# Optimization experiments

Hardware: AMD Instinct MI355X
Metric: run time of the kernel (lower is better)

The kernel has to match this reference:

```python
import jax, jax.numpy as jnp
import numpy as np


def setup_inputs() -> dict:
    key = jax.random.key(0)
    k1, k2 = jax.random.split(key)
    B, HW, C, M, P = 8, 4096, 1024, 32, 512
    feature_map = jax.random.normal(k1, (B, HW, C), dtype=jnp.float32)
    # normalized (y, x) coords in [0,1], as produced by mask.nonzero()/[H,W]
    point_coords = jax.random.uniform(k2, (B, M, P, 2), dtype=jnp.float32)
    return {"feature_map": feature_map, "point_coords": point_coords}


def reference(feature_map, point_coords):
    # feature_map: [B, H*W, C]; point_coords: [B, M, P, 2] as (y_norm, x_norm).
    B, HW, C = feature_map.shape
    h = w = int(np.sqrt(HW))
    # torch flips coords to (x, y); grid_sample(align_corners=True) maps
    # grid g = 2*coord-1 to pixel coord*(size-1).
    y = point_coords[..., 0] * (h - 1)  # [B, M, P]
    x = point_coords[..., 1] * (w - 1)
    x0f = jnp.floor(x)
    y0f = jnp.floor(y)
    wx = (x - x0f)[..., None]  # [B, M, P, 1]
    wy = (y - y0f)[..., None]
    ix0 = jnp.clip(x0f.astype(jnp.int32), 0, w - 1)
    ix1 = jnp.clip(ix0 + 1, 0, w - 1)
    iy0 = jnp.clip(y0f.astype(jnp.int32), 0, h - 1)
    iy1 = jnp.clip(iy0 + 1, 0, h - 1)

    def gather(iy, ix):
        idx = (iy * w + ix).reshape(B, -1)  # [B, M*P]
        g = jnp.take_along_axis(feature_map, idx[:, :, None], axis=1)  # [B, M*P, C]
        return g.reshape(B, iy.shape[1], iy.shape[2], C)

    f00 = gather(iy0, ix0)
    f01 = gather(iy0, ix1)
    f10 = gather(iy1, ix0)
    f11 = gather(iy1, ix1)
    # bilinear interpolation -> [B, M, P, C]
    sampled = (f00 * (1 - wx) * (1 - wy) + f01 * wx * (1 - wy)
               + f10 * (1 - wx) * wy + f11 * wx * wy)
    # AdaptiveAvgPool1d(1) over points, then transpose -> [B, M, 1, C]
    region_feat = jnp.mean(sampled, axis=2, keepdims=True)
    return region_feat
```

## Files before the change

kernel.cpp:

```cpp
#include <hip/hip_runtime.h>


#define NB 8
#define NM 32
#define NP 512
#define NC 1024
#define NH 64
#define NHW 4096

#define KC    128
#define NKC   (NHW / KC)
#define CPT   8
#define MT    8
#define CTILE 512
#define NCT   (NC / CTILE)
#define PF    4

__global__ __launch_bounds__(256) void scatter_w(
    const float* __restrict__ pc, float* __restrict__ W)
{
    int idx = blockIdx.x * 256 + threadIdx.x;
    int bm  = idx >> 9;
    int m   = bm & (NM - 1);
    int b   = bm >> 5;

    float2 c = ((const float2*)pc)[idx];
    float y = c.x * 63.0f;
    float x = c.y * 63.0f;
    float x0f = floorf(x), y0f = floorf(y);
    float wx = x - x0f, wy = y - y0f;
    int ix0 = min(max((int)x0f, 0), 63);
    int ix1 = min(ix0 + 1, 63);
    int iy0 = min(max((int)y0f, 0), 63);
    int iy1 = min(iy0 + 1, 63);
    float wx1 = 1.0f - wx, wy1 = 1.0f - wy;
    const float s = 1.0f / (float)NP;

    float* Wb = W + (size_t)b * (NHW * NM) + m;
    atomicAdd(Wb + ((iy0 * NH + ix0) * NM), wx1 * wy1 * s);
    atomicAdd(Wb + ((iy0 * NH + ix1) * NM), wx  * wy1 * s);
    atomicAdd(Wb + ((iy1 * NH + ix0) * NM), wx1 * wy  * s);
    atomicAdd(Wb + ((iy1 * NH + ix1) * NM), wx  * wy  * s);
}

__global__ __launch_bounds__(256, 2) void wgemm(
    const float* __restrict__ W, const float* __restrict__ F,
    float* __restrict__ P)
{
    __shared__ float sW[KC * NM];

    const int kc   = blockIdx.x;
    const int ct   = blockIdx.y;
    const int b    = blockIdx.z;
    const int tid  = threadIdx.x;
    const int mq   = tid >> 6;
    const int lane = tid & 63;
    const int c0   = ct * CTILE + lane * CPT;
    const int hw0  = kc * KC;

    {
        const float4* Wg = (const float4*)(W + ((size_t)b * NHW + hw0) * NM);
        float4* sW4 = (float4*)sW;
#pragma unroll
        for (int j = 0; j < 4; ++j)
            sW4[tid + 256 * j] = Wg[tid + 256 * j];
    }
    __syncthreads();

    const float4* __restrict__ Fb =
        (const float4*)(F + ((size_t)b * NHW + hw0) * NC + c0);
    const int fstride = NC / 4;

    float4 acc[MT][2];
#pragma unroll
    for (int m = 0; m < MT; ++m) {
        acc[m][0] = make_float4(0.f, 0.f, 0.f, 0.f);
        acc[m][1] = make_float4(0.f, 0.f, 0.f, 0.f);
    }

    float4 fbuf[PF][2];
#pragma unroll
    for (int j = 0; j < PF; ++j) {
        fbuf[j][0] = Fb[(size_t)j * fstride];
        fbuf[j][1] = Fb[(size_t)j * fstride + 1];
    }

    const float4* sWq = (const float4*)(sW + mq * MT);

    for (int i = 0; i < KC; i += PF) {
#pragma unroll
        for (int j = 0; j < PF; ++j) {
            const int s = i + j;
            float4 wa0 = sWq[(size_t)s * (NM / 4)];
            float4 wa1 = sWq[(size_t)s * (NM / 4) + 1];

            float4 f0 = fbuf[j][0];
            float4 f1 = fbuf[j][1];
            if (i + PF < KC) {
                fbuf[j][0] = Fb[(size_t)(s + PF) * fstride];
                fbuf[j][1] = Fb[(size_t)(s + PF) * fstride + 1];
            }

            const float wm[MT] = { wa0.x, wa0.y, wa0.z, wa0.w,
                                   wa1.x, wa1.y, wa1.z, wa1.w };
#pragma unroll
            for (int m = 0; m < MT; ++m) {
                float w = wm[m];
                acc[m][0].x = fmaf(w, f0.x, acc[m][0].x);
                acc[m][0].y = fmaf(w, f0.y, acc[m][0].y);
                acc[m][0].z = fmaf(w, f0.z, acc[m][0].z);
                acc[m][0].w = fmaf(w, f0.w, acc[m][0].w);
                acc[m][1].x = fmaf(w, f1.x, acc[m][1].x);
                acc[m][1].y = fmaf(w, f1.y, acc[m][1].y);
                acc[m][1].z = fmaf(w, f1.z, acc[m][1].z);
                acc[m][1].w = fmaf(w, f1.w, acc[m][1].w);
            }
        }
    }

    float* pb = P + (((size_t)kc * NB + b) * NM + mq * MT) * NC + c0;
#pragma unroll
    for (int mm = 0; mm < MT; ++mm) {
        ((float4*)(pb + (size_t)mm * NC))[0] = acc[mm][0];
        ((float4*)(pb + (size_t)mm * NC))[1] = acc[mm][1];
    }
}

__global__ __launch_bounds__(256) void reduce_p(
    const float* __restrict__ P, float* __restrict__ out)
{
    const int idx = blockIdx.x * 256 + threadIdx.x;
    const float4* p4 = (const float4*)P;
    const int stride = NB * NM * NC / 4;
    float4 s = make_float4(0.f, 0.f, 0.f, 0.f);
#pragma unroll
    for (int kc = 0; kc < NKC; ++kc) {
        float4 v = p4[(size_t)kc * stride + idx];
        s.x += v.x; s.y += v.y; s.z += v.z; s.w += v.w;
    }
    ((float4*)out)[idx] = s;
}

__global__ __launch_bounds__(256) void region_pool_direct(
    const float* __restrict__ fm, const float* __restrict__ pc,
    float* __restrict__ out)
{
    __shared__ int4   sIdx[NP];
    __shared__ float4 sWt[NP];
    const int bid = blockIdx.x;
    const int b   = bid >> 5;
    const int tid = threadIdx.x;
    const float2* pc2 = (const float2*)(pc + (size_t)bid * NP * 2);
    for (int p = tid; p < NP; p += 256) {
        float2 c = pc2[p];
        float y = c.x * 63.0f, x = c.y * 63.0f;
        float x0f = floorf(x), y0f = floorf(y);
        float wx = x - x0f, wy = y - y0f;
        int ix0 = min(max((int)x0f, 0), 63);
        int ix1 = min(ix0 + 1, 63);
        int iy0 = min(max((int)y0f, 0), 63);
        int iy1 = min(iy0 + 1, 63);
        sIdx[p] = make_int4((iy0 * NH + ix0) << 10, (iy0 * NH + ix1) << 10,
                            (iy1 * NH + ix0) << 10, (iy1 * NH + ix1) << 10);
        float wx1 = 1.0f - wx, wy1 = 1.0f - wy;
        sWt[p] = make_float4(wx1 * wy1, wx * wy1, wx1 * wy, wx * wy);
    }
    __syncthreads();
    const float* Fb = fm + (size_t)b * (NHW * NC) + tid * 4;
    float4 acc = make_float4(0.f, 0.f, 0.f, 0.f);
#pragma unroll 4
    for (int p = 0; p < NP; ++p) {
        int4 off = sIdx[p]; float4 w = sWt[p];
        float4 f00 = *(const float4*)(Fb + off.x);
        float4 f01 = *(const float4*)(Fb + off.y);
        float4 f10 = *(const float4*)(Fb + off.z);
        float4 f11 = *(const float4*)(Fb + off.w);
        acc.x = fmaf(w.x, f00.x, fmaf(w.y, f01.x, fmaf(w.z, f10.x, fmaf(w.w, f11.x, acc.x))));
        acc.y = fmaf(w.x, f00.y, fmaf(w.y, f01.y, fmaf(w.z, f10.y, fmaf(w.w, f11.y, acc.y))));
        acc.z = fmaf(w.x, f00.z, fmaf(w.y, f01.z, fmaf(w.z, f10.z, fmaf(w.w, f11.z, acc.z))));
        acc.w = fmaf(w.x, f00.w, fmaf(w.y, f01.w, fmaf(w.z, f10.w, fmaf(w.w, f11.w, acc.w))));
    }
    const float inv = 1.0f / (float)NP;
    ((float4*)(out + (size_t)bid * NC))[tid] =
        make_float4(acc.x * inv, acc.y * inv, acc.z * inv, acc.w * inv);
}

extern "C" void kernel_launch(void* const* d_in, const int* in_sizes, int n_in,
                              void* d_out, int out_size, void* d_ws, size_t ws_size,
                              hipStream_t stream) {
    const float* fm = (const float*)d_in[0];
    const float* pc = (const float*)d_in[1];
    float* out = (float*)d_out;

    const size_t wbytes = (size_t)NB * NHW * NM * sizeof(float);
    const size_t pbytes = (size_t)NKC * NB * NM * NC * sizeof(float);
    if (ws_size >= wbytes + pbytes) {
        float* W = (float*)d_ws;
        float* P = (float*)((char*)d_ws + wbytes);
        hipMemsetAsync(W, 0, wbytes, stream);
        scatter_w<<<(NB * NM * NP) / 256, 256, 0, stream>>>(pc, W);
        dim3 grid(NKC, NCT, NB);
        wgemm<<<grid, 256, 0, stream>>>(W, fm, P);
        reduce_p<<<(NB * NM * NC / 4) / 256, 256, 0, stream>>>(P, out);
    } else {
        region_pool_direct<<<NB * NM, 256, 0, stream>>>(fm, pc, out);
    }
}
```

Baseline: 250.3 us.

## Stage feature tiles in LDS with async global-to-LDS loads, double buffered

In the weighted-GEMM kernel, all four wavefronts of a block previously loaded the same feature rows straight from global memory into registers. Each block now copies chunks of eight feature rows into a shared double-buffered LDS tile using the global_load_lds builtin, with each wavefront fetching two rows. The copy of the next chunk overlaps compute on the current one. Columns are now interleaved (lane*4 and 256+lane*4) so the LDS reads are contiguous. This removes the redundant global/L1 traffic, at the cost of a block barrier per chunk and reliance on correct wait handling for the async LDS loads.

```diff
diff --git a/kernel.cpp b/kernel.cpp
--- a/kernel.cpp
+++ b/kernel.cpp
@@ -8,13 +8,13 @@
 #define NH 64
 #define NHW 4096
 
-#define KC    128
-#define NKC   (NHW / KC)
-#define CPT   8
-#define MT    8
-#define CTILE 512
-#define NCT   (NC / CTILE)
-#define PF    4
+#define KC     128
+#define NKC    (NHW / KC)
+#define MT     8
+#define CTILE  512
+#define NCT    (NC / CTILE)
+#define G      8
+#define NCHUNK (KC / G)
 
 __global__ __launch_bounds__(256) void scatter_w(
     const float* __restrict__ pc, float* __restrict__ W)
@@ -43,11 +43,30 @@
     atomicAdd(Wb + ((iy1 * NH + ix1) * NM), wx  * wy  * s);
 }
 
+__device__ __forceinline__ void dma_rows(const float* src, float* dstBase,
+                                         int lane)
+{
+#pragma unroll
+    for (int jj = 0; jj < 2; ++jj) {
+        const float* s0 = src + jj * NC + lane * 4;
+        const float* s1 = src + jj * NC + 256 + lane * 4;
+        float* d0 = dstBase + jj * CTILE + lane * 4;
+        float* d1 = dstBase + jj * CTILE + 256 + lane * 4;
+        __builtin_amdgcn_global_load_lds(
+            (const __attribute__((address_space(1))) void*)s0,
+            (__attribute__((address_space(3))) void*)d0, 16, 0, 0);
+        __builtin_amdgcn_global_load_lds(
+            (const __attribute__((address_space(1))) void*)s1,
+            (__attribute__((address_space(3))) void*)d1, 16, 0, 0);
+    }
+}
+
 __global__ __launch_bounds__(256, 2) void wgemm(
     const float* __restrict__ W, const float* __restrict__ F,
     float* __restrict__ P)
 {
     __shared__ float sW[KC * NM];
+    __shared__ float sF[2][G][CTILE];
 
     const int kc   = blockIdx.x;
     const int ct   = blockIdx.y;
@@ -55,7 +74,6 @@
     const int tid  = threadIdx.x;
     const int mq   = tid >> 6;
     const int lane = tid & 63;
-    const int c0   = ct * CTILE + lane * CPT;
     const int hw0  = kc * KC;
 
     {
@@ -65,11 +83,11 @@
         for (int j = 0; j < 4; ++j)
             sW4[tid + 256 * j] = Wg[tid + 256 * j];
     }
+
+    const float* Fbase = F + ((size_t)b * NHW + hw0) * NC + ct * CTILE;
+
+    dma_rows(Fbase + (size_t)(mq * 2) * NC, &sF[0][mq * 2][0], lane);
     __syncthreads();
-
-    const float4* __restrict__ Fb =
-        (const float4*)(F + ((size_t)b * NHW + hw0) * NC + c0);
-    const int fstride = NC / 4;
 
     float4 acc[MT][2];
 #pragma unroll
@@ -78,31 +96,21 @@
         acc[m][1] = make_float4(0.f, 0.f, 0.f, 0.f);
     }
 
-    float4 fbuf[PF][2];
-#pragma unroll
-    for (int j = 0; j < PF; ++j) {
-        fbuf[j][0] = Fb[(size_t)j * fstride];
-        fbuf[j][1] = Fb[(size_t)j * fstride + 1];
-    }
-
-    const float4* sWq = (const float4*)(sW + mq * MT);
-
-    for (int i = 0; i < KC; i += PF) {
-#pragma unroll
-        for (int j = 0; j < PF; ++j) {
-            const int s = i + j;
-            float4 wa0 = sWq[(size_t)s * (NM / 4)];
-            float4 wa1 = sWq[(size_t)s * (NM / 4) + 1];
-
-            float4 f0 = fbuf[j][0];
-            float4 f1 = fbuf[j][1];
-            if (i + PF < KC) {
-                fbuf[j][0] = Fb[(size_t)(s + PF) * fstride];
-                fbuf[j][1] = Fb[(size_t)(s + PF) * fstride + 1];
-            }
-
-            const float wm[MT] = { wa0.x, wa0.y, wa0.z, wa0.w,
-                                   wa1.x, wa1.y, wa1.z, wa1.w };
+    int buf = 0;
+    for (int t = 0; t < NCHUNK; ++t) {
+        if (t + 1 < NCHUNK)
+            dma_rows(Fbase + (size_t)((t + 1) * G + mq * 2) * NC,
+                     &sF[buf ^ 1][mq * 2][0], lane);
+
+        const float* sWrow = sW + (t * G) * NM + mq * MT;
+#pragma unroll
+        for (int j = 0; j < G; ++j) {
+            float4 w0 = *(const float4*)(sWrow + j * NM);
+            float4 w1 = *(const float4*)(sWrow + j * NM + 4);
+            float4 f0 = *(const float4*)(&sF[buf][j][4 * lane]);
+            float4 f1 = *(const float4*)(&sF[buf][j][256 + 4 * lane]);
+            const float wm[MT] = { w0.x, w0.y, w0.z, w0.w,
+                                   w1.x, w1.y, w1.z, w1.w };
 #pragma unroll
             for (int m = 0; m < MT; ++m) {
                 float w = wm[m];
@@ -116,13 +124,15 @@
                 acc[m][1].w = fmaf(w, f1.w, acc[m][1].w);
             }
         }
-    }
-
-    float* pb = P + (((size_t)kc * NB + b) * NM + mq * MT) * NC + c0;
+        __syncthreads();
+        buf ^= 1;
+    }
+
+    float* pb = P + (((size_t)kc * NB + b) * NM + mq * MT) * NC + ct * CTILE;
 #pragma unroll
     for (int mm = 0; mm < MT; ++mm) {
-        ((float4*)(pb + (size_t)mm * NC))[0] = acc[mm][0];
-        ((float4*)(pb + (size_t)mm * NC))[1] = acc[mm][1];
+        *(float4*)(pb + (size_t)mm * NC + 4 * lane)       = acc[mm][0];
+        *(float4*)(pb + (size_t)mm * NC + 256 + 4 * lane) = acc[mm][1];
     }
 }
 
```

Measured after the change: 233.4 us. -6.7%, faster.

## Narrow wgemm to one float4 per thread, deeper prefetch, higher occupancy

Applied to the files above, without the earlier changes.

Each wgemm thread now handles 4 channels instead of 8, with the channel tile halved to 256. This doubles the grid and halves the accumulator registers, so launch bounds target 4 waves per SIMD. Coalesced loads now cover contiguous float4 per lane, and the prefetch depth rises to 8 rows with a peeled tail instead of a branch inside the loop. The cost is that each shared-memory weight read now feeds half as many FMAs, and the feature rows are streamed by twice as many blocks.

```diff
diff --git a/kernel.cpp b/kernel.cpp
--- a/kernel.cpp
+++ b/kernel.cpp
@@ -10,11 +10,11 @@
 
 #define KC    128
 #define NKC   (NHW / KC)
-#define CPT   8
 #define MT    8
-#define CTILE 512
+#define CTILE 256
 #define NCT   (NC / CTILE)
-#define PF    4
+#define PF    8
+#define FS4   (NC / 4)
 
 __global__ __launch_bounds__(256) void scatter_w(
     const float* __restrict__ pc, float* __restrict__ W)
@@ -43,7 +43,7 @@
     atomicAdd(Wb + ((iy1 * NH + ix1) * NM), wx  * wy  * s);
 }
 
-__global__ __launch_bounds__(256, 2) void wgemm(
+__global__ __launch_bounds__(256, 4) void wgemm(
     const float* __restrict__ W, const float* __restrict__ F,
     float* __restrict__ P)
 {
@@ -55,7 +55,6 @@
     const int tid  = threadIdx.x;
     const int mq   = tid >> 6;
     const int lane = tid & 63;
-    const int c0   = ct * CTILE + lane * CPT;
     const int hw0  = kc * KC;
 
     {
@@ -68,62 +67,61 @@
     __syncthreads();
 
     const float4* __restrict__ Fb =
-        (const float4*)(F + ((size_t)b * NHW + hw0) * NC + c0);
-    const int fstride = NC / 4;
-
-    float4 acc[MT][2];
-#pragma unroll
-    for (int m = 0; m < MT; ++m) {
-        acc[m][0] = make_float4(0.f, 0.f, 0.f, 0.f);
-        acc[m][1] = make_float4(0.f, 0.f, 0.f, 0.f);
-    }
-
-    float4 fbuf[PF][2];
-#pragma unroll
-    for (int j = 0; j < PF; ++j) {
-        fbuf[j][0] = Fb[(size_t)j * fstride];
-        fbuf[j][1] = Fb[(size_t)j * fstride + 1];
-    }
-
-    const float4* sWq = (const float4*)(sW + mq * MT);
-
-    for (int i = 0; i < KC; i += PF) {
+        (const float4*)(F + ((size_t)b * NHW + hw0) * NC + ct * CTILE) + lane;
+
+    float4 acc[MT];
+#pragma unroll
+    for (int m = 0; m < MT; ++m) acc[m] = make_float4(0.f, 0.f, 0.f, 0.f);
+
+    float4 r[PF];
+#pragma unroll
+    for (int j = 0; j < PF; ++j) r[j] = Fb[j * FS4];
+
+    const float* sWq = sW + mq * MT;
+
+    for (int t = 0; t < KC - PF; t += PF) {
 #pragma unroll
         for (int j = 0; j < PF; ++j) {
-            const int s = i + j;
-            float4 wa0 = sWq[(size_t)s * (NM / 4)];
-            float4 wa1 = sWq[(size_t)s * (NM / 4) + 1];
-
-            float4 f0 = fbuf[j][0];
-            float4 f1 = fbuf[j][1];
-            if (i + PF < KC) {
-                fbuf[j][0] = Fb[(size_t)(s + PF) * fstride];
-                fbuf[j][1] = Fb[(size_t)(s + PF) * fstride + 1];
-            }
-
-            const float wm[MT] = { wa0.x, wa0.y, wa0.z, wa0.w,
-                                   wa1.x, wa1.y, wa1.z, wa1.w };
+            float4 f = r[j];
+            r[j] = Fb[(t + j + PF) * FS4];
+            const float* wr = sWq + (t + j) * NM;
+            float4 w0 = *(const float4*)(wr);
+            float4 w1 = *(const float4*)(wr + 4);
+            const float wm[MT] = { w0.x, w0.y, w0.z, w0.w,
+                                   w1.x, w1.y, w1.z, w1.w };
 #pragma unroll
             for (int m = 0; m < MT; ++m) {
                 float w = wm[m];
-                acc[m][0].x = fmaf(w, f0.x, acc[m][0].x);
-                acc[m][0].y = fmaf(w, f0.y, acc[m][0].y);
-                acc[m][0].z = fmaf(w, f0.z, acc[m][0].z);
-                acc[m][0].w = fmaf(w, f0.w, acc[m][0].w);
-                acc[m][1].x = fmaf(w, f1.x, acc[m][1].x);
-                acc[m][1].y = fmaf(w, f1.y, acc[m][1].y);
-                acc[m][1].z = fmaf(w, f1.z, acc[m][1].z);
-                acc[m][1].w = fmaf(w, f1.w, acc[m][1].w);
+                acc[m].x = fmaf(w, f.x, acc[m].x);
+                acc[m].y = fmaf(w, f.y, acc[m].y);
+                acc[m].z = fmaf(w, f.z, acc[m].z);
+                acc[m].w = fmaf(w, f.w, acc[m].w);
             }
         }
     }
-
-    float* pb = P + (((size_t)kc * NB + b) * NM + mq * MT) * NC + c0;
-#pragma unroll
-    for (int mm = 0; mm < MT; ++mm) {
-        ((float4*)(pb + (size_t)mm * NC))[0] = acc[mm][0];
-        ((float4*)(pb + (size_t)mm * NC))[1] = acc[mm][1];
-    }
+#pragma unroll
+    for (int j = 0; j < PF; ++j) {
+        float4 f = r[j];
+        const float* wr = sWq + (KC - PF + j) * NM;
+        float4 w0 = *(const float4*)(wr);
+        float4 w1 = *(const float4*)(wr + 4);
+        const float wm[MT] = { w0.x, w0.y, w0.z, w0.w,
+                               w1.x, w1.y, w1.z, w1.w };
+#pragma unroll
+        for (int m = 0; m < MT; ++m) {
+            float w = wm[m];
+            acc[m].x = fmaf(w, f.x, acc[m].x);
+            acc[m].y = fmaf(w, f.y, acc[m].y);
+            acc[m].z = fmaf(w, f.z, acc[m].z);
+            acc[m].w = fmaf(w, f.w, acc[m].w);
+        }
+    }
+
+    float* pb = P + (((size_t)kc * NB + b) * NM + mq * MT) * NC
+              + ct * CTILE + 4 * lane;
+#pragma unroll
+    for (int mm = 0; mm < MT; ++mm)
+        *(float4*)(pb + (size_t)mm * NC) = acc[mm];
 }
 
 __global__ __launch_bounds__(256) void reduce_p(
```

New measurement: 236.5 us. -5.5%, faster.
